# Optimization experiments

Hardware: AMD Instinct MI355X
Metric: run time of the kernel (lower is better)

Reference implementation:

```python
import jax, jax.numpy as jnp
import numpy as np

ALPHA = 0.2  # LeakyReLU negative slope
NEG_INF = jnp.float32(-9e15)


def setup_inputs() -> dict:
    key = jax.random.key(0)
    k1, k2, k3, k4, k5, k6 = jax.random.split(key, 6)
    B, N, F_in, F_out = 8, 2048, 256, 64
    h = jax.random.normal(k1, (B, N, F_in), dtype=jnp.float32)
    adj = jax.random.randint(k2, (B, N, N), 0, 2, dtype=jnp.int32)
    level = jax.random.uniform(k3, (B, N), dtype=jnp.float32)
    node_type = jax.random.uniform(k4, (B, N, N), dtype=jnp.float32)
    W = jax.random.normal(k5, (F_in, F_out), dtype=jnp.float32) * 1.414 / np.sqrt(F_in)
    a = jax.random.normal(k6, (2 * F_out, 1), dtype=jnp.float32) * 1.414 / np.sqrt(2 * F_out)
    return {"h": h, "adj": adj, "level": level, "node_type": node_type, "W": W, "a": a}


def reference(h, adj, level, node_type, W, a):
    # h: [B,N,Fin], adj/node_type: [B,N,N], level: [B,N], W: [Fin,Fout], a: [2*Fout,1]
    F_out = W.shape[1]
    Wh = jnp.einsum('bnf,fo->bno', h, W)  # [B,N,Fout]
    # Additive attention decomposed: e[b,i,j] = a1.Wh_i + a2.Wh_j (no O(N^2*2F) tensor)
    a1 = a[:F_out, 0]
    a2 = a[F_out:, 0]
    f1 = Wh @ a1  # [B,N]
    f2 = Wh @ a2  # [B,N]
    e = jax.nn.leaky_relu(f1[:, :, None] + f2[:, None, :], negative_slope=ALPHA)  # [B,N,N]
    # gat_our=True path: node_type scales scores, level scales Wh
    e = e * node_type
    Wh = Wh * level[:, :, None]
    attention = jnp.where(adj > 0, e, NEG_INF)
    attention = jax.nn.softmax(attention, axis=1)  # faithful: original softmax over dim=1
    # dropout p=0 / eval mode -> identity
    h_prime = jnp.einsum('bij,bjo->bio', attention, Wh)  # [B,N,Fout]
    return jax.nn.relu(h_prime)  # concat=True
```

## Files before the change

kernel.cpp:

```cpp
#include <hip/hip_runtime.h>

#define BB 8
#define NN 2048
#define FIN 256
#define FO 64

typedef short short8_t __attribute__((ext_vector_type(8)));
typedef float float4_t __attribute__((ext_vector_type(4)));

__device__ __forceinline__ unsigned short f2bf(float x) {
  unsigned int u = __float_as_uint(x);
  unsigned int r = (u + 0x7fffu + ((u >> 16) & 1u)) >> 16;
  return (unsigned short)r;
}

__global__ __launch_bounds__(256) void k0_zero(float* __restrict__ scol) {
  scol[blockIdx.x * 256 + threadIdx.x] = 0.0f;
}

__global__ __launch_bounds__(256) void k1_gemm(
    const float* __restrict__ h,
    const float* __restrict__ level,
    const float* __restrict__ W,
    const float* __restrict__ a,
    float* __restrict__ V, float* __restrict__ f1, float* __restrict__ f2)
{
  __shared__ float hs[16 * 260];
  __shared__ float parts1[16 * 17];
  __shared__ float parts2[16 * 17];
  int t = threadIdx.x;
  int b = blockIdx.x >> 7;
  int i0 = (blockIdx.x & 127) * 16;

  {
    int r_ld = t >> 4, f0 = (t & 15) * 16;
    const float* hp = h + (size_t)(b * NN + i0 + r_ld) * FIN + f0;
    float4 x0 = *(const float4*)(hp);
    float4 x1 = *(const float4*)(hp + 4);
    float4 x2 = *(const float4*)(hp + 8);
    float4 x3 = *(const float4*)(hp + 12);
    float* hd = &hs[r_ld * 260 + f0];
    *(float4*)(hd + 0) = x0; *(float4*)(hd + 4) = x1;
    *(float4*)(hd + 8) = x2; *(float4*)(hd + 12) = x3;
  }
  __syncthreads();

  int r = t >> 4;
  int c4 = (t & 15) * 4;
  float4 acc = {0, 0, 0, 0};

  for (int f = 0; f < FIN; f += 8) {
    float4 hv0 = *(const float4*)&hs[r * 260 + f];
    float4 hv1 = *(const float4*)&hs[r * 260 + f + 4];
    float hvv[8] = {hv0.x, hv0.y, hv0.z, hv0.w, hv1.x, hv1.y, hv1.z, hv1.w};
    #pragma unroll
    for (int k = 0; k < 8; ++k) {
      float4 wv = *(const float4*)&W[(size_t)(f + k) * FO + c4];
      acc.x += hvv[k] * wv.x; acc.y += hvv[k] * wv.y;
      acc.z += hvv[k] * wv.z; acc.w += hvv[k] * wv.w;
    }
  }

  float p1 = acc.x * a[c4] + acc.y * a[c4 + 1] + acc.z * a[c4 + 2] + acc.w * a[c4 + 3];
  float p2 = acc.x * a[64 + c4] + acc.y * a[64 + c4 + 1] +
             acc.z * a[64 + c4 + 2] + acc.w * a[64 + c4 + 3];
  parts1[r * 17 + (t & 15)] = p1;
  parts2[r * 17 + (t & 15)] = p2;
  __syncthreads();
  if (t < 16) {
    float s1 = 0.f, s2 = 0.f;
    #pragma unroll
    for (int g = 0; g < 16; ++g) { s1 += parts1[t * 17 + g]; s2 += parts2[t * 17 + g]; }
    f1[b * NN + i0 + t] = s1;
    f2[b * NN + i0 + t] = s2;
  }

  float lv = level[b * NN + i0 + r];
  float4 vv = {acc.x * lv, acc.y * lv, acc.z * lv, acc.w * lv};
  *(float4*)&V[(size_t)(b * NN + i0 + r) * FO + c4] = vv;
}

template <int STORE_U>
__global__ __launch_bounds__(512) void k2a_stats(
    const int* __restrict__ adj,
    const float* __restrict__ ntp,
    const float* __restrict__ f1,
    const float* __restrict__ f2,
    unsigned short* __restrict__ u_bf,
    unsigned char* __restrict__ bits,
    float* __restrict__ scol)
{
  __shared__ float red[512 * 9];
  int t = threadIdx.x;
  int blk = blockIdx.x;
  int chunk = blk >> 8;
  int b = (blk >> 5) & 7;
  int jt = blk & 31;
  int j0 = jt * 64;
  int tj = t & 7, isub = t >> 3;
  int j8 = j0 + tj * 8;

  float4 f2lo = *(const float4*)(f2 + b * NN + j8);
  float4 f2hi = *(const float4*)(f2 + b * NN + j8 + 4);
  float f2v[8] = {f2lo.x, f2lo.y, f2lo.z, f2lo.w, f2hi.x, f2hi.y, f2hi.z, f2hi.w};

  int4 A0[4], A1[4];
  float4 Nv0[4], Nv1[4];
  float F1[4];
  #pragma unroll
  for (int ii = 0; ii < 4; ++ii) {
    size_t base = (size_t)(b * NN + chunk * 256 + ii * 64 + isub);
    const int* ap = adj + base * NN + j8;
    A0[ii] = *(const int4*)ap;
    A1[ii] = *(const int4*)(ap + 4);
    const float* npp = ntp + base * NN + j8;
    Nv0[ii] = *(const float4*)npp;
    Nv1[ii] = *(const float4*)(npp + 4);
    F1[ii] = f1[base];
  }

  float acc8[8] = {0, 0, 0, 0, 0, 0, 0, 0};
  #pragma unroll
  for (int ii = 0; ii < 4; ++ii) {
    size_t base = (size_t)(b * NN + chunk * 256 + ii * 64 + isub);
    float f1v = F1[ii];
    float ntf[8] = {Nv0[ii].x, Nv0[ii].y, Nv0[ii].z, Nv0[ii].w,
                    Nv1[ii].x, Nv1[ii].y, Nv1[ii].z, Nv1[ii].w};
    int am[8] = {A0[ii].x, A0[ii].y, A0[ii].z, A0[ii].w,
                 A1[ii].x, A1[ii].y, A1[ii].z, A1[ii].w};
    float uv[8];
    unsigned int mb = 0;
    #pragma unroll
    for (int e = 0; e < 8; ++e) {
      float x = f1v + f2v[e];
      x = fmaxf(x, 0.2f * x);
      float E = x * ntf[e];
      bool m = am[e] > 0;
      float u = m ? __expf(E) : 0.0f;
      uv[e] = u;
      acc8[e] += u;
      mb |= (m ? 1u : 0u) << e;
    }
    if (STORE_U) {
      uint4 pk;
      pk.x = (unsigned int)f2bf(uv[0]) | ((unsigned int)f2bf(uv[1]) << 16);
      pk.y = (unsigned int)f2bf(uv[2]) | ((unsigned int)f2bf(uv[3]) << 16);
      pk.z = (unsigned int)f2bf(uv[4]) | ((unsigned int)f2bf(uv[5]) << 16);
      pk.w = (unsigned int)f2bf(uv[6]) | ((unsigned int)f2bf(uv[7]) << 16);
      *(uint4*)(u_bf + base * NN + j8) = pk;
    } else {
      bits[base * (NN / 8) + jt * 8 + tj] = (unsigned char)mb;
    }
  }

  #pragma unroll
  for (int e = 0; e < 8; ++e) red[t * 9 + e] = acc8[e];
  __syncthreads();
  if (t < 64) {
    int tjj = t >> 3, ee = t & 7;
    float s = 0.f;
    for (int is = 0; is < 64; ++is) s += red[(is * 8 + tjj) * 9 + ee];
    atomicAdd(&scol[b * NN + j0 + t], s);
  }
}

__global__ __launch_bounds__(256) void k2b_pack(
    const float* __restrict__ V,
    const float* __restrict__ scol,
    unsigned short* __restrict__ vf)
{
  int t = threadIdx.x;
  int b = blockIdx.x >> 6;
  int kk = blockIdx.x & 63;
  int ng = t >> 6;
  int l = t & 63;
  int jb = kk * 32 + ((l >> 4) * 8);
  int o = ng * 16 + (l & 15);
  unsigned int pk[4];
  #pragma unroll
  for (int p = 0; p < 4; ++p) {
    int jr0 = jb + 2 * p, jr1 = jb + 2 * p + 1;
    float s0 = scol[b * NN + jr0];
    float s1 = scol[b * NN + jr1];
    float i0 = (s0 > 0.f) ? (1.0f / s0) : 0.0f;
    float i1 = (s1 > 0.f) ? (1.0f / s1) : 0.0f;
    float v0 = V[(size_t)(b * NN + jr0) * FO + o] * i0;
    float v1 = V[(size_t)(b * NN + jr1) * FO + o] * i1;
    pk[p] = (unsigned int)f2bf(v0) | ((unsigned int)f2bf(v1) << 16);
  }
  *(uint4*)(vf + (size_t)(((b * 64 + kk) * 4 + ng) * 64 + l) * 8) =
      make_uint4(pk[0], pk[1], pk[2], pk[3]);
}

__global__ __launch_bounds__(256) void k3_agg_u(
    const unsigned short* __restrict__ u_bf,
    const unsigned short* __restrict__ vf,
    float* __restrict__ outp)
{
  __shared__ float red[4 * 16 * 68];
  int t = threadIdx.x;
  int b = blockIdx.x >> 7;
  int i0 = (blockIdx.x & 127) * 16;
  int w = t >> 6, l = t & 63;
  int col = l & 15, quad = l >> 4;
  const unsigned short* urow = u_bf + (size_t)(b * NN + i0 + col) * NN + quad * 8;
  const unsigned short* vbase = vf + (size_t)(b * 64) * 2048 + l * 8;

  short8_t Aall[16];
  #pragma unroll
  for (int s = 0; s < 16; ++s)
    Aall[s] = *(const short8_t*)(urow + (size_t)(w * 16 + s) * 32);

  const unsigned short* vb0 = vbase + (size_t)(w * 16) * 2048;
  short8_t c0 = *(const short8_t*)(vb0);
  short8_t c1 = *(const short8_t*)(vb0 + 512);
  short8_t c2 = *(const short8_t*)(vb0 + 1024);
  short8_t c3 = *(const short8_t*)(vb0 + 1536);

  float4_t acc0 = {0, 0, 0, 0}, acc1 = {0, 0, 0, 0}, acc2 = {0, 0, 0, 0}, acc3 = {0, 0, 0, 0};

  #pragma unroll
  for (int s = 0; s < 16; ++s) {
    short8_t n0, n1, n2, n3;
    if (s < 15) {
      const unsigned short* vn = vbase + (size_t)(w * 16 + s + 1) * 2048;
      n0 = *(const short8_t*)(vn);
      n1 = *(const short8_t*)(vn + 512);
      n2 = *(const short8_t*)(vn + 1024);
      n3 = *(const short8_t*)(vn + 1536);
    }
    acc0 = __builtin_amdgcn_mfma_f32_16x16x32_bf16(Aall[s], c0, acc0, 0, 0, 0);
    acc1 = __builtin_amdgcn_mfma_f32_16x16x32_bf16(Aall[s], c1, acc1, 0, 0, 0);
    acc2 = __builtin_amdgcn_mfma_f32_16x16x32_bf16(Aall[s], c2, acc2, 0, 0, 0);
    acc3 = __builtin_amdgcn_mfma_f32_16x16x32_bf16(Aall[s], c3, acc3, 0, 0, 0);
    if (s < 15) { c0 = n0; c1 = n1; c2 = n2; c3 = n3; }
  }

  #pragma unroll
  for (int r = 0; r < 4; ++r) {
    int rowi = quad * 4 + r;
    red[w * 1088 + rowi * 68 + 0 + col] = acc0[r];
    red[w * 1088 + rowi * 68 + 16 + col] = acc1[r];
    red[w * 1088 + rowi * 68 + 32 + col] = acc2[r];
    red[w * 1088 + rowi * 68 + 48 + col] = acc3[r];
  }
  __syncthreads();

  int row = t >> 4, o4 = (t & 15) * 4;
  const float* rp = &red[row * 68 + o4];
  float4 s0 = *(const float4*)(rp);
  float4 s1 = *(const float4*)(rp + 1088);
  float4 s2 = *(const float4*)(rp + 2176);
  float4 s3 = *(const float4*)(rp + 3264);
  float4 o;
  o.x = fmaxf(s0.x + s1.x + s2.x + s3.x, 0.0f);
  o.y = fmaxf(s0.y + s1.y + s2.y + s3.y, 0.0f);
  o.z = fmaxf(s0.z + s1.z + s2.z + s3.z, 0.0f);
  o.w = fmaxf(s0.w + s1.w + s2.w + s3.w, 0.0f);
  *(float4*)&outp[(size_t)(b * NN + i0 + row) * FO + o4] = o;
}

__global__ __launch_bounds__(256) void k3_agg_b(
    const float* __restrict__ ntp,
    const unsigned char* __restrict__ bits,
    const float* __restrict__ f1,
    const float* __restrict__ f2,
    const unsigned short* __restrict__ vf,
    float* __restrict__ outp)
{
  __shared__ float red[4 * 16 * 68];
  int t = threadIdx.x;
  int b = blockIdx.x >> 7;
  int i0 = (blockIdx.x & 127) * 16;
  int w = t >> 6, l = t & 63;
  int col = l & 15, quad = l >> 4;
  int gi = b * NN + i0 + col;
  float f1v = f1[gi];
  const float* ntrow = ntp + (size_t)gi * NN;
  const unsigned char* brow = bits + (size_t)gi * (NN / 8);
  float4_t acc0 = {0, 0, 0, 0}, acc1 = {0, 0, 0, 0}, acc2 = {0, 0, 0, 0}, acc3 = {0, 0, 0, 0};

  for (int s = 0; s < 16; ++s) {
    int kk = w * 16 + s;
    int jq = kk * 32 + quad * 8;
    unsigned int m8 = brow[jq >> 3];
    float4 n0 = *(const float4*)(ntrow + jq);
    float4 n1 = *(const float4*)(ntrow + jq + 4);
    float4 g0 = *(const float4*)(f2 + b * NN + jq);
    float4 g1 = *(const float4*)(f2 + b * NN + jq + 4);
    float f2v[8] = {g0.x, g0.y, g0.z, g0.w, g1.x, g1.y, g1.z, g1.w};
    float ntf[8] = {n0.x, n0.y, n0.z, n0.w, n1.x, n1.y, n1.z, n1.w};
    union { unsigned int u[4]; short8_t v; } A;
    #pragma unroll
    for (int p = 0; p < 4; ++p) {
      int e0 = 2 * p, e1 = 2 * p + 1;
      float x0 = f1v + f2v[e0]; x0 = fmaxf(x0, 0.2f * x0);
      float u0 = ((m8 >> e0) & 1u) ? __expf(x0 * ntf[e0]) : 0.0f;
      float x1 = f1v + f2v[e1]; x1 = fmaxf(x1, 0.2f * x1);
      float u1 = ((m8 >> e1) & 1u) ? __expf(x1 * ntf[e1]) : 0.0f;
      A.u[p] = (unsigned int)f2bf(u0) | ((unsigned int)f2bf(u1) << 16);
    }
    const unsigned short* vb = vf + (size_t)(b * 64 + kk) * 2048 + l * 8;
    short8_t bf0 = *(const short8_t*)(vb);
    short8_t bf1 = *(const short8_t*)(vb + 512);
    short8_t bf2 = *(const short8_t*)(vb + 1024);
    short8_t bf3 = *(const short8_t*)(vb + 1536);
    acc0 = __builtin_amdgcn_mfma_f32_16x16x32_bf16(A.v, bf0, acc0, 0, 0, 0);
    acc1 = __builtin_amdgcn_mfma_f32_16x16x32_bf16(A.v, bf1, acc1, 0, 0, 0);
    acc2 = __builtin_amdgcn_mfma_f32_16x16x32_bf16(A.v, bf2, acc2, 0, 0, 0);
    acc3 = __builtin_amdgcn_mfma_f32_16x16x32_bf16(A.v, bf3, acc3, 0, 0, 0);
  }

  #pragma unroll
  for (int r = 0; r < 4; ++r) {
    int rowi = quad * 4 + r;
    red[w * 1088 + rowi * 68 + 0 + col] = acc0[r];
    red[w * 1088 + rowi * 68 + 16 + col] = acc1[r];
    red[w * 1088 + rowi * 68 + 32 + col] = acc2[r];
    red[w * 1088 + rowi * 68 + 48 + col] = acc3[r];
  }
  __syncthreads();

  int row = t >> 4, o4 = (t & 15) * 4;
  const float* rp = &red[row * 68 + o4];
  float4 s0 = *(const float4*)(rp);
  float4 s1 = *(const float4*)(rp + 1088);
  float4 s2 = *(const float4*)(rp + 2176);
  float4 s3 = *(const float4*)(rp + 3264);
  float4 o;
  o.x = fmaxf(s0.x + s1.x + s2.x + s3.x, 0.0f);
  o.y = fmaxf(s0.y + s1.y + s2.y + s3.y, 0.0f);
  o.z = fmaxf(s0.z + s1.z + s2.z + s3.z, 0.0f);
  o.w = fmaxf(s0.w + s1.w + s2.w + s3.w, 0.0f);
  *(float4*)&outp[(size_t)(b * NN + i0 + row) * FO + o4] = o;
}

extern "C" void kernel_launch(void* const* d_in, const int* in_sizes, int n_in,
                              void* d_out, int out_size, void* d_ws, size_t ws_size,
                              hipStream_t stream) {
  const float* h = (const float*)d_in[0];
  const int* adj = (const int*)d_in[1];
  const float* level = (const float*)d_in[2];
  const float* ntm = (const float*)d_in[3];
  const float* W = (const float*)d_in[4];
  const float* a = (const float*)d_in[5];
  float* outp = (float*)d_out;

  float* V = (float*)d_ws;
  float* f1 = V + (size_t)BB * NN * FO;
  float* f2 = f1 + BB * NN;
  float* scol = f2 + BB * NN;
  unsigned short* vf = (unsigned short*)(scol + BB * NN);
  char* tail = (char*)(vf + (size_t)BB * NN * FO);
  size_t fixed = (size_t)(tail - (char*)d_ws);
  size_t need_u = fixed + (size_t)BB * NN * NN * 2;
  bool big = (ws_size >= need_u);

  k0_zero<<<64, 256, 0, stream>>>(scol);
  k1_gemm<<<1024, 256, 0, stream>>>(h, level, W, a, V, f1, f2);
  if (big) {
    unsigned short* u_bf = (unsigned short*)tail;
    k2a_stats<1><<<2048, 512, 0, stream>>>(adj, ntm, f1, f2, u_bf, nullptr, scol);
    k2b_pack<<<512, 256, 0, stream>>>(V, scol, vf);
    k3_agg_u<<<1024, 256, 0, stream>>>(u_bf, vf, outp);
  } else {
    unsigned char* bits = (unsigned char*)tail;
    k2a_stats<0><<<2048, 512, 0, stream>>>(adj, ntm, f1, f2, nullptr, bits, scol);
    k2b_pack<<<512, 256, 0, stream>>>(V, scol, vf);
    k3_agg_b<<<1024, 256, 0, stream>>>(ntm, bits, f1, f2, vf, outp);
  }
}
```

Baseline: 376.7 us.

## Retile stats kernel so each block sweeps full rows of eight nodes

The column-stats kernel now gives each 256-thread block 8 rows of one batch and has it sweep all 2048 columns in four 512-wide chunks, replacing the old 256-row by 64-column tiles. Each wave reads 32 contiguous bytes per lane across a 2 KB row segment, where before each block touched short 256-byte strips across many rows. The cross-row reduction shrinks to 4 waves per chunk, at the cost of more atomicAdds to scol (2048 columns per block) and two barriers per chunk.

```diff
diff --git a/kernel.cpp b/kernel.cpp
--- a/kernel.cpp
+++ b/kernel.cpp
@@ -81,7 +81,7 @@
 }
 
 template <int STORE_U>
-__global__ __launch_bounds__(512) void k2a_stats(
+__global__ __launch_bounds__(256) void k2a_stats(
     const int* __restrict__ adj,
     const float* __restrict__ ntp,
     const float* __restrict__ f1,
@@ -90,77 +90,72 @@
     unsigned char* __restrict__ bits,
     float* __restrict__ scol)
 {
-  __shared__ float red[512 * 9];
-  int t = threadIdx.x;
-  int blk = blockIdx.x;
-  int chunk = blk >> 8;
-  int b = (blk >> 5) & 7;
-  int jt = blk & 31;
-  int j0 = jt * 64;
-  int tj = t & 7, isub = t >> 3;
-  int j8 = j0 + tj * 8;
-
-  float4 f2lo = *(const float4*)(f2 + b * NN + j8);
-  float4 f2hi = *(const float4*)(f2 + b * NN + j8 + 4);
-  float f2v[8] = {f2lo.x, f2lo.y, f2lo.z, f2lo.w, f2hi.x, f2hi.y, f2hi.z, f2hi.w};
-
-  int4 A0[4], A1[4];
-  float4 Nv0[4], Nv1[4];
-  float F1[4];
-  #pragma unroll
-  for (int ii = 0; ii < 4; ++ii) {
-    size_t base = (size_t)(b * NN + chunk * 256 + ii * 64 + isub);
-    const int* ap = adj + base * NN + j8;
-    A0[ii] = *(const int4*)ap;
-    A1[ii] = *(const int4*)(ap + 4);
-    const float* npp = ntp + base * NN + j8;
-    Nv0[ii] = *(const float4*)npp;
-    Nv1[ii] = *(const float4*)(npp + 4);
-    F1[ii] = f1[base];
-  }
-
-  float acc8[8] = {0, 0, 0, 0, 0, 0, 0, 0};
-  #pragma unroll
-  for (int ii = 0; ii < 4; ++ii) {
-    size_t base = (size_t)(b * NN + chunk * 256 + ii * 64 + isub);
-    float f1v = F1[ii];
-    float ntf[8] = {Nv0[ii].x, Nv0[ii].y, Nv0[ii].z, Nv0[ii].w,
-                    Nv1[ii].x, Nv1[ii].y, Nv1[ii].z, Nv1[ii].w};
-    int am[8] = {A0[ii].x, A0[ii].y, A0[ii].z, A0[ii].w,
-                 A1[ii].x, A1[ii].y, A1[ii].z, A1[ii].w};
-    float uv[8];
-    unsigned int mb = 0;
-    #pragma unroll
-    for (int e = 0; e < 8; ++e) {
-      float x = f1v + f2v[e];
-      x = fmaxf(x, 0.2f * x);
-      float E = x * ntf[e];
-      bool m = am[e] > 0;
-      float u = m ? __expf(E) : 0.0f;
-      uv[e] = u;
-      acc8[e] += u;
-      mb |= (m ? 1u : 0u) << e;
-    }
-    if (STORE_U) {
-      uint4 pk;
-      pk.x = (unsigned int)f2bf(uv[0]) | ((unsigned int)f2bf(uv[1]) << 16);
-      pk.y = (unsigned int)f2bf(uv[2]) | ((unsigned int)f2bf(uv[3]) << 16);
-      pk.z = (unsigned int)f2bf(uv[4]) | ((unsigned int)f2bf(uv[5]) << 16);
-      pk.w = (unsigned int)f2bf(uv[6]) | ((unsigned int)f2bf(uv[7]) << 16);
-      *(uint4*)(u_bf + base * NN + j8) = pk;
-    } else {
-      bits[base * (NN / 8) + jt * 8 + tj] = (unsigned char)mb;
-    }
-  }
-
-  #pragma unroll
-  for (int e = 0; e < 8; ++e) red[t * 9 + e] = acc8[e];
-  __syncthreads();
-  if (t < 64) {
-    int tjj = t >> 3, ee = t & 7;
-    float s = 0.f;
-    for (int is = 0; is < 64; ++is) s += red[(is * 8 + tjj) * 9 + ee];
-    atomicAdd(&scol[b * NN + j0 + t], s);
+  __shared__ float red[4 * 520];
+  int t = threadIdx.x;
+  int b = blockIdx.x >> 8;
+  int i0 = (blockIdx.x & 255) * 8;
+  int w = t >> 6, l = t & 63;
+
+  #pragma unroll
+  for (int c = 0; c < 4; ++c) {
+    int j8 = c * 512 + l * 8;
+    float4 f2lo = *(const float4*)(f2 + b * NN + j8);
+    float4 f2hi = *(const float4*)(f2 + b * NN + j8 + 4);
+    float f2v[8] = {f2lo.x, f2lo.y, f2lo.z, f2lo.w, f2hi.x, f2hi.y, f2hi.z, f2hi.w};
+    float acc8[8] = {0, 0, 0, 0, 0, 0, 0, 0};
+
+    #pragma unroll
+    for (int r = 0; r < 2; ++r) {
+      size_t base = (size_t)(b * NN + i0 + w * 2 + r);
+      const int* ap = adj + base * NN + j8;
+      int4 a0 = *(const int4*)ap;
+      int4 a1 = *(const int4*)(ap + 4);
+      const float* npp = ntp + base * NN + j8;
+      float4 n0 = *(const float4*)npp;
+      float4 n1 = *(const float4*)(npp + 4);
+      float f1v = f1[base];
+      float ntf[8] = {n0.x, n0.y, n0.z, n0.w, n1.x, n1.y, n1.z, n1.w};
+      int am[8] = {a0.x, a0.y, a0.z, a0.w, a1.x, a1.y, a1.z, a1.w};
+      float uv[8];
+      unsigned int mb = 0;
+      #pragma unroll
+      for (int e = 0; e < 8; ++e) {
+        float x = f1v + f2v[e];
+        x = fmaxf(x, 0.2f * x);
+        float E = x * ntf[e];
+        bool m = am[e] > 0;
+        float u = m ? __expf(E) : 0.0f;
+        uv[e] = u;
+        acc8[e] += u;
+        mb |= (m ? 1u : 0u) << e;
+      }
+      if (STORE_U) {
+        uint4 pk;
+        pk.x = (unsigned int)f2bf(uv[0]) | ((unsigned int)f2bf(uv[1]) << 16);
+        pk.y = (unsigned int)f2bf(uv[2]) | ((unsigned int)f2bf(uv[3]) << 16);
+        pk.z = (unsigned int)f2bf(uv[4]) | ((unsigned int)f2bf(uv[5]) << 16);
+        pk.w = (unsigned int)f2bf(uv[6]) | ((unsigned int)f2bf(uv[7]) << 16);
+        *(uint4*)(u_bf + base * NN + j8) = pk;
+      } else {
+        bits[base * (NN / 8) + c * 64 + l] = (unsigned char)mb;
+      }
+    }
+
+    #pragma unroll
+    for (int e = 0; e < 8; ++e) red[w * 520 + l * 8 + e] = acc8[e];
+    __syncthreads();
+    {
+      int j2 = t * 2;
+      float s0 = 0.f, s1 = 0.f;
+      #pragma unroll
+      for (int ww = 0; ww < 4; ++ww) {
+        float2 v = *(const float2*)&red[ww * 520 + j2];
+        s0 += v.x; s1 += v.y;
+      }
+      atomicAdd(&scol[b * NN + c * 512 + j2], s0);
+      atomicAdd(&scol[b * NN + c * 512 + j2 + 1], s1);
+    }
+    __syncthreads();
   }
 }
 
@@ -360,12 +355,12 @@
   k1_gemm<<<1024, 256, 0, stream>>>(h, level, W, a, V, f1, f2);
   if (big) {
     unsigned short* u_bf = (unsigned short*)tail;
-    k2a_stats<1><<<2048, 512, 0, stream>>>(adj, ntm, f1, f2, u_bf, nullptr, scol);
+    k2a_stats<1><<<2048, 256, 0, stream>>>(adj, ntm, f1, f2, u_bf, nullptr, scol);
     k2b_pack<<<512, 256, 0, stream>>>(V, scol, vf);
     k3_agg_u<<<1024, 256, 0, stream>>>(u_bf, vf, outp);
   } else {
     unsigned char* bits = (unsigned char*)tail;
-    k2a_stats<0><<<2048, 512, 0, stream>>>(adj, ntm, f1, f2, nullptr, bits, scol);
+    k2a_stats<0><<<2048, 256, 0, stream>>>(adj, ntm, f1, f2, nullptr, bits, scol);
     k2b_pack<<<512, 256, 0, stream>>>(V, scol, vf);
     k3_agg_b<<<1024, 256, 0, stream>>>(ntm, bits, f1, f2, vf, outp);
   }
```

Result: no change. 379.8 us (+0.8%).
